# Optimization experiments

Hardware: AMD Instinct MI355X
Metric: run time of the kernel (lower is better)

## Reference

```python
import jax, jax.numpy as jnp
import numpy as np

E = 6            # number of residual adapter experts / event groups
MAX_SCALE = 0.05
RESIDUAL_SCALE = 1.0
EPS = 1e-12      # F.normalize eps


def setup_inputs() -> dict:
    key = jax.random.key(0)
    ks = jax.random.split(key, 8)
    B, L, D, H, T = 4, 1024, 768, 1536, 32
    seq_embeddings = jax.random.normal(ks[0], (B, L, D), dtype=jnp.float32)
    next_type_ids = jax.random.randint(ks[1], (B, L), 0, T, dtype=jnp.int32)
    # Adapter bank params (6 two-layer MLPs). Original zero-inits W2/b2; we use
    # small random values so the math is exercised.
    W1 = jax.random.normal(ks[2], (E, D, H), dtype=jnp.float32) * 0.02
    b1 = jax.random.normal(ks[3], (E, H), dtype=jnp.float32) * 0.02
    W2 = jax.random.normal(ks[4], (E, H, D), dtype=jnp.float32) * 0.02
    b2 = jax.random.normal(ks[5], (E, D), dtype=jnp.float32) * 0.02
    raw_alpha = jnp.full((E,), -4.0, dtype=jnp.float32)
    # build_event_type_to_group_tensor stand-in: event type -> one of 6 groups
    event_type_to_group = (jnp.arange(T, dtype=jnp.int32) % E)
    return {"seq_embeddings": seq_embeddings, "next_type_ids": next_type_ids,
            "W1": W1, "b1": b1, "W2": W2, "b2": b2,
            "raw_alpha": raw_alpha, "event_type_to_group": event_type_to_group}


def reference(seq_embeddings, next_type_ids, W1, b1, W2, b2, raw_alpha, event_type_to_group):
    x = seq_embeddings                                  # [B, L, D]
    T = event_type_to_group.shape[0]
    safe = jnp.clip(next_type_ids.astype(jnp.int32), 0, T - 1)
    group_ids = event_type_to_group[safe]               # [B, L] in [0, 6)
    # Dense compute of all 6 adapters (dropout is identity in eval mode)
    h = jax.nn.relu(jnp.einsum('bld,edh->bleh', x, W1) + b1)   # [B, L, 6, H]
    residuals = jnp.einsum('bleh,ehd->bled', h, W2) + b2       # [B, L, 6, D]
    # Gather the chosen expert's residual per token
    idx = group_ids[..., None, None]                           # [B, L, 1, 1]
    residual = jnp.take_along_axis(residuals, idx, axis=2)[:, :, 0, :]  # [B, L, D]
    alpha_all = MAX_SCALE * jax.nn.sigmoid(raw_alpha)          # [6]
    alpha = alpha_all[group_ids][..., None]                    # [B, L, 1]
    out = x + RESIDUAL_SCALE * alpha * residual
    norm = jnp.linalg.norm(out, axis=-1, keepdims=True)
    out = out / jnp.maximum(norm, EPS)
    return out
```

## Files before the change

### kernel.cpp

```cpp
#include <hip/hip_runtime.h>
#include <hip/hip_bf16.h>
#include <stdint.h>

#define NTOK 4096
#define DDIM 768
#define HDIM 1536
#define NEXP 6
#define NTYPE 32
#define PADROWS 4224
#define MAXTILES 70

typedef __bf16 bf16x8 __attribute__((ext_vector_type(8)));
typedef float f32x4 __attribute__((ext_vector_type(4)));

static __device__ __forceinline__ unsigned short f2bf(float f) {
  union { float f; unsigned u; } v; v.f = f;
  unsigned r = v.u + 0x7FFFu + ((v.u >> 16) & 1u);
  return (unsigned short)(r >> 16);
}

static __device__ __forceinline__ void gload_lds16(const void* g, void* lds) {
  auto* g1 = reinterpret_cast<const __attribute__((address_space(1))) uint32_t*>(
      reinterpret_cast<uintptr_t>(g));
  auto* l3 = reinterpret_cast<__attribute__((address_space(3))) uint32_t*>(
      (uint32_t)reinterpret_cast<uintptr_t>(lds));
  __builtin_amdgcn_global_load_lds(g1, l3, 16, 0, 0);
}

__global__ __launch_bounds__(256)
void prep_kernel(const float* __restrict__ W1, const float* __restrict__ W2,
                 unsigned short* __restrict__ w1t, unsigned short* __restrict__ w2t,
                 const int* __restrict__ ids, const int* __restrict__ ev2g,
                 int* __restrict__ perm, int* __restrict__ meta) {
  const int z = blockIdx.z;
  const int t = threadIdx.x;
  if (z == 12) {
    if (blockIdx.x != 0 || blockIdx.y != 0) return;
    __shared__ int s_ev2g[NTYPE];
    __shared__ int s_cnt[NEXP];
    __shared__ int s_off[NEXP];
    __shared__ int s_cur[NEXP];
    if (t < NTYPE) s_ev2g[t] = ev2g[t];
    if (t < NEXP) { s_cnt[t] = 0; s_cur[t] = 0; }
    __syncthreads();
    int g[16];
    #pragma unroll
    for (int i = 0; i < 16; ++i) {
      int idx = t * 16 + i;
      int ty = ids[idx];
      ty = ty < 0 ? 0 : (ty > NTYPE - 1 ? NTYPE - 1 : ty);
      g[i] = s_ev2g[ty];
      atomicAdd(&s_cnt[g[i]], 1);
    }
    __syncthreads();
    if (t == 0) {
      int off = 0, nt = 0;
      int* table = meta + 21;
      for (int e = 0; e < NEXP; ++e) {
        s_off[e] = off;
        int c = s_cnt[e];
        for (int k = 0; k * 64 < c; ++k) {
          int rem = c - k * 64;
          table[nt * 3 + 0] = e;
          table[nt * 3 + 1] = off + k * 64;
          table[nt * 3 + 2] = rem < 64 ? rem : 64;
          ++nt;
        }
        off += c;
      }
      meta[20] = nt;
    }
    __syncthreads();
    #pragma unroll
    for (int i = 0; i < 16; ++i) {
      int idx = t * 16 + i;
      int pos = s_off[g[i]] + atomicAdd(&s_cur[g[i]], 1);
      perm[pos] = idx;
    }
    return;
  }
  __shared__ float tile[64][65];
  const float* src;
  unsigned short* dst;
  int R, C, bx, by;
  if (z < 6) {
    src = W1 + (size_t)z * 768 * 1536; dst = w1t + (size_t)z * 768 * 1536;
    R = 768; C = 1536; bx = blockIdx.x; by = blockIdx.y;
  } else {
    src = W2 + (size_t)(z - 6) * 768 * 1536; dst = w2t + (size_t)(z - 6) * 768 * 1536;
    R = 1536; C = 768; bx = blockIdx.y; by = blockIdx.x;
  }
  const int r0 = by * 64, c0 = bx * 64;
  const int lr = t >> 4;
  const int lc = (t & 15) << 2;
  #pragma unroll
  for (int i = 0; i < 4; ++i) {
    float4 v = *reinterpret_cast<const float4*>(src + (size_t)(r0 + i * 16 + lr) * C + c0 + lc);
    tile[i * 16 + lr][lc]     = v.x;
    tile[i * 16 + lr][lc + 1] = v.y;
    tile[i * 16 + lr][lc + 2] = v.z;
    tile[i * 16 + lr][lc + 3] = v.w;
  }
  __syncthreads();
  const int l8 = (t & 7) << 3;
  #pragma unroll
  for (int p = 0; p < 2; ++p) {
    int j = p * 32 + (t >> 3);
    union { unsigned short u[8]; uint4 v; } pk;
    #pragma unroll
    for (int k = 0; k < 8; ++k) pk.u[k] = f2bf(tile[l8 + k][j]);
    *reinterpret_cast<uint4*>(dst + (size_t)(c0 + j) * R + r0 + l8) = pk.v;
  }
}

__global__ __launch_bounds__(256)
void xgather_kernel(const float* __restrict__ x, const int* __restrict__ perm,
                    unsigned short* __restrict__ xg) {
  const int wave = threadIdx.x >> 6, lane = threadIdx.x & 63;
  const int row = (blockIdx.x << 2) + wave;
  const int src = perm[row];
  const float4* in = reinterpret_cast<const float4*>(x + (size_t)src * DDIM);
  ushort4* outp = reinterpret_cast<ushort4*>(xg + (size_t)row * DDIM);
  #pragma unroll
  for (int j = 0; j < 3; ++j) {
    float4 v = in[lane + j * 64];
    ushort4 o;
    o.x = f2bf(v.x); o.y = f2bf(v.y); o.z = f2bf(v.z); o.w = f2bf(v.w);
    outp[lane + j * 64] = o;
  }
}

template <int K, int NT, bool PASS2>
__global__ __launch_bounds__(256, 3)
void gemm_kernel(const unsigned short* __restrict__ A,
                 const unsigned short* __restrict__ Bw,
                 const float* __restrict__ bias,
                 const int* __restrict__ meta,
                 const int* __restrict__ perm,
                 const float* __restrict__ x,
                 const float* __restrict__ raw_alpha,
                 unsigned short* __restrict__ hout,
                 float* __restrict__ out)
{
  constexpr int BM = 64, BN = 128;
  constexpr int NDIM = NT * BN;
  constexpr int NK = K / 64;

  const int nwg = MAXTILES * NT;
  const int q = nwg >> 3, r = nwg & 7;
  const int x8 = blockIdx.x & 7;
  const int o8 = blockIdx.x >> 3;
  const int vid = (x8 < r ? x8 * (q + 1) : r * (q + 1) + (x8 - r) * q) + o8;
  const int nt = vid / MAXTILES;
  const int mt = vid % MAXTILES;
  if (mt >= meta[20]) return;
  const int* table = meta + 21;
  const int e = table[mt * 3 + 0], base = table[mt * 3 + 1], cnt = table[mt * 3 + 2];

  __shared__ __align__(16) unsigned short As[2][BM * 64];
  __shared__ __align__(16) unsigned short Bs[2][BN * 64];

  const int tid = threadIdx.x;
  const int wave = tid >> 6, lane = tid & 63;
  const int wm = wave >> 1, wn = wave & 1;

  const unsigned short* Abase = A + (size_t)base * K;
  const unsigned short* Bbase = Bw + ((size_t)e * NDIM + (size_t)nt * BN) * K;

  f32x4 acc[2][4];
  #pragma unroll
  for (int i = 0; i < 2; ++i)
    #pragma unroll
    for (int j = 0; j < 4; ++j) acc[i][j] = (f32x4){0.f, 0.f, 0.f, 0.f};

  int aRow[2], aElem[2], aLds[2];
  #pragma unroll
  for (int i = 0; i < 2; ++i) {
    int chunk = i * 256 + tid;
    int o = chunk * 16;
    int row = o >> 7;
    int inb = (o & 127) ^ ((row & 7) << 4);
    aRow[i] = row; aElem[i] = inb >> 1;
    aLds[i] = (i * 256 + wave * 64) * 16;
  }
  int bRow[4], bElem[4], bLds[4];
  #pragma unroll
  for (int i = 0; i < 4; ++i) {
    int chunk = i * 256 + tid;
    int o = chunk * 16;
    int row = o >> 7;
    int inb = (o & 127) ^ ((row & 7) << 4);
    bRow[i] = row; bElem[i] = inb >> 1;
    bLds[i] = (i * 256 + wave * 64) * 16;
  }

  #pragma unroll
  for (int i = 0; i < 2; ++i)
    gload_lds16(Abase + (size_t)aRow[i] * K + aElem[i], (char*)As[0] + aLds[i]);
  #pragma unroll
  for (int i = 0; i < 4; ++i)
    gload_lds16(Bbase + (size_t)bRow[i] * K + bElem[i], (char*)Bs[0] + bLds[i]);
  __syncthreads();

  int cur = 0;
  for (int kt = 0; kt < NK; ++kt) {
    if (kt + 1 < NK) {
      const int k0 = (kt + 1) * 64;
      #pragma unroll
      for (int i = 0; i < 2; ++i)
        gload_lds16(Abase + (size_t)aRow[i] * K + k0 + aElem[i], (char*)As[cur ^ 1] + aLds[i]);
      #pragma unroll
      for (int i = 0; i < 4; ++i)
        gload_lds16(Bbase + (size_t)bRow[i] * K + k0 + bElem[i], (char*)Bs[cur ^ 1] + bLds[i]);
    }
    #pragma unroll
    for (int ks = 0; ks < 2; ++ks) {
      bf16x8 av[2], bv[4];
      const int kb = ks * 64 + ((lane >> 4) << 4);
      #pragma unroll
      for (int mi = 0; mi < 2; ++mi) {
        int row = wm * 32 + mi * 16 + (lane & 15);
        int byte = (row * 128 + kb) ^ ((row & 7) << 4);
        av[mi] = *reinterpret_cast<const bf16x8*>((const char*)As[cur] + byte);
      }
      #pragma unroll
      for (int nj = 0; nj < 4; ++nj) {
        int row = wn * 64 + nj * 16 + (lane & 15);
        int byte = (row * 128 + kb) ^ ((row & 7) << 4);
        bv[nj] = *reinterpret_cast<const bf16x8*>((const char*)Bs[cur] + byte);
      }
      #pragma unroll
      for (int mi = 0; mi < 2; ++mi)
        #pragma unroll
        for (int nj = 0; nj < 4; ++nj)
          acc[mi][nj] = __builtin_amdgcn_mfma_f32_16x16x32_bf16(av[mi], bv[nj], acc[mi][nj], 0, 0, 0);
    }
    __syncthreads();
    cur ^= 1;
  }

  const int col0 = nt * BN + wn * 64;
  if constexpr (!PASS2) {
    #pragma unroll
    for (int nj = 0; nj < 4; ++nj) {
      int n = col0 + nj * 16 + (lane & 15);
      float bv = bias[e * NDIM + n];
      #pragma unroll
      for (int mi = 0; mi < 2; ++mi) {
        int rbase = wm * 32 + mi * 16 + ((lane >> 4) << 2);
        #pragma unroll
        for (int rr = 0; rr < 4; ++rr) {
          int row = rbase + rr;
          if (row < cnt) {
            float v = fmaxf(acc[mi][nj][rr] + bv, 0.0f);
            hout[(size_t)(base + row) * NDIM + n] = f2bf(v);
          }
        }
      }
    }
  } else {
    float alpha = 0.05f / (1.0f + expf(-raw_alpha[e]));
    #pragma unroll
    for (int nj = 0; nj < 4; ++nj) {
      int n = col0 + nj * 16 + (lane & 15);
      float bv = bias[e * NDIM + n];
      #pragma unroll
      for (int mi = 0; mi < 2; ++mi) {
        int rbase = wm * 32 + mi * 16 + ((lane >> 4) << 2);
        #pragma unroll
        for (int rr = 0; rr < 4; ++rr) {
          int row = rbase + rr;
          if (row < cnt) {
            int tok = perm[base + row];
            size_t oi = (size_t)tok * DDIM + n;
            out[oi] = x[oi] + alpha * (acc[mi][nj][rr] + bv);
          }
        }
      }
    }
  }
}

__global__ __launch_bounds__(256)
void norm_kernel(float* __restrict__ out) {
  const int wave = threadIdx.x >> 6, lane = threadIdx.x & 63;
  const int tok = (blockIdx.x << 2) + wave;
  float4* p = reinterpret_cast<float4*>(out) + (size_t)tok * 192;
  float4 a = p[lane], b = p[lane + 64], c = p[lane + 128];
  float ss = a.x * a.x + a.y * a.y + a.z * a.z + a.w * a.w
           + b.x * b.x + b.y * b.y + b.z * b.z + b.w * b.w
           + c.x * c.x + c.y * c.y + c.z * c.z + c.w * c.w;
  #pragma unroll
  for (int off = 32; off; off >>= 1) ss += __shfl_xor(ss, off);
  const float s = 1.0f / fmaxf(sqrtf(ss), 1e-12f);
  a.x *= s; a.y *= s; a.z *= s; a.w *= s;
  b.x *= s; b.y *= s; b.z *= s; b.w *= s;
  c.x *= s; c.y *= s; c.z *= s; c.w *= s;
  p[lane] = a; p[lane + 64] = b; p[lane + 128] = c;
}


extern "C" void kernel_launch(void* const* d_in, const int* in_sizes, int n_in,
                              void* d_out, int out_size, void* d_ws, size_t ws_size,
                              hipStream_t stream) {
  const float* x      = (const float*)d_in[0];
  const int*   ids    = (const int*)d_in[1];
  const float* W1     = (const float*)d_in[2];
  const float* b1     = (const float*)d_in[3];
  const float* W2     = (const float*)d_in[4];
  const float* b2     = (const float*)d_in[5];
  const float* ralpha = (const float*)d_in[6];
  const int*   ev2g   = (const int*)d_in[7];
  float* out = (float*)d_out;
  char* ws = (char*)d_ws;

  unsigned short* w1t = (unsigned short*)(ws);
  unsigned short* w2t = (unsigned short*)(ws + 14155776);
  unsigned short* xg  = (unsigned short*)(ws + 28311552);
  unsigned short* h   = (unsigned short*)(ws + 34799616);
  int* perm = (int*)(ws + 47775744);
  int* meta = (int*)(ws + 47808512);

  prep_kernel<<<dim3(24, 12, 13), 256, 0, stream>>>(W1, W2, w1t, w2t, ids, ev2g, perm, meta);
  xgather_kernel<<<1024, 256, 0, stream>>>(x, perm, xg);
  gemm_kernel<DDIM, 12, false><<<MAXTILES * 12, 256, 0, stream>>>(
      xg, w1t, b1, meta, perm, x, ralpha, h, out);
  gemm_kernel<HDIM, 6, true><<<MAXTILES * 6, 256, 0, stream>>>(
      h, w2t, b2, meta, perm, x, ralpha, nullptr, out);
  norm_kernel<<<1024, 256, 0, stream>>>(out);
}
```

Measured before the change: 186.2 us.

## Triple-buffer GEMM LDS tiles with explicit vmcnt waits for deeper prefetch

Converts the double-buffered global-to-LDS pipeline in the expert GEMM into a three-stage ring that prefetches two K tiles ahead. Manual s_waitcnt vmcnt counts and raw s_barrier calls replace __syncthreads, so the kernel waits only for the tile about to be consumed. This is meant to hide more global load latency behind MFMA work. In exchange, LDS use per block grows by half and the occupancy hint drops from 3 to 2 blocks per CU. The hard-coded vmcnt values assume exactly six loads per stage.

```diff
diff --git a/kernel.cpp b/kernel.cpp
--- a/kernel.cpp
+++ b/kernel.cpp
@@ -131,7 +131,7 @@
 }
 
 template <int K, int NT, bool PASS2>
-__global__ __launch_bounds__(256, 3)
+__global__ __launch_bounds__(256, 2)
 void gemm_kernel(const unsigned short* __restrict__ A,
                  const unsigned short* __restrict__ Bw,
                  const float* __restrict__ bias,
@@ -157,8 +157,8 @@
   const int* table = meta + 21;
   const int e = table[mt * 3 + 0], base = table[mt * 3 + 1], cnt = table[mt * 3 + 2];
 
-  __shared__ __align__(16) unsigned short As[2][BM * 64];
-  __shared__ __align__(16) unsigned short Bs[2][BN * 64];
+  __shared__ __align__(16) unsigned short As[3][BM * 64];
+  __shared__ __align__(16) unsigned short Bs[3][BN * 64];
 
   const int tid = threadIdx.x;
   const int wave = tid >> 6, lane = tid & 63;
@@ -194,25 +194,28 @@
     bLds[i] = (i * 256 + wave * 64) * 16;
   }
 
-  #pragma unroll
-  for (int i = 0; i < 2; ++i)
-    gload_lds16(Abase + (size_t)aRow[i] * K + aElem[i], (char*)As[0] + aLds[i]);
-  #pragma unroll
-  for (int i = 0; i < 4; ++i)
-    gload_lds16(Bbase + (size_t)bRow[i] * K + bElem[i], (char*)Bs[0] + bLds[i]);
-  __syncthreads();
-
-  int cur = 0;
+  auto stage = [&](int kt, int buf) {
+    const int k0 = kt * 64;
+    #pragma unroll
+    for (int i = 0; i < 2; ++i)
+      gload_lds16(Abase + (size_t)aRow[i] * K + k0 + aElem[i], (char*)As[buf] + aLds[i]);
+    #pragma unroll
+    for (int i = 0; i < 4; ++i)
+      gload_lds16(Bbase + (size_t)bRow[i] * K + k0 + bElem[i], (char*)Bs[buf] + bLds[i]);
+  };
+
+  stage(0, 0);
+  stage(1, 1);
+
+  int get = 0, put = 2;
   for (int kt = 0; kt < NK; ++kt) {
-    if (kt + 1 < NK) {
-      const int k0 = (kt + 1) * 64;
-      #pragma unroll
-      for (int i = 0; i < 2; ++i)
-        gload_lds16(Abase + (size_t)aRow[i] * K + k0 + aElem[i], (char*)As[cur ^ 1] + aLds[i]);
-      #pragma unroll
-      for (int i = 0; i < 4; ++i)
-        gload_lds16(Bbase + (size_t)bRow[i] * K + k0 + bElem[i], (char*)Bs[cur ^ 1] + bLds[i]);
-    }
+    if (kt + 2 < NK) stage(kt + 2, put);
+    __builtin_amdgcn_sched_barrier(0);
+    if (kt + 2 < NK)      asm volatile("s_waitcnt vmcnt(12)" ::: "memory");
+    else if (kt + 1 < NK) asm volatile("s_waitcnt vmcnt(6)" ::: "memory");
+    else                  asm volatile("s_waitcnt vmcnt(0)" ::: "memory");
+    __builtin_amdgcn_s_barrier();
+    __builtin_amdgcn_sched_barrier(0);
     #pragma unroll
     for (int ks = 0; ks < 2; ++ks) {
       bf16x8 av[2], bv[4];
@@ -221,13 +224,13 @@
       for (int mi = 0; mi < 2; ++mi) {
         int row = wm * 32 + mi * 16 + (lane & 15);
         int byte = (row * 128 + kb) ^ ((row & 7) << 4);
-        av[mi] = *reinterpret_cast<const bf16x8*>((const char*)As[cur] + byte);
+        av[mi] = *reinterpret_cast<const bf16x8*>((const char*)As[get] + byte);
       }
       #pragma unroll
       for (int nj = 0; nj < 4; ++nj) {
         int row = wn * 64 + nj * 16 + (lane & 15);
         int byte = (row * 128 + kb) ^ ((row & 7) << 4);
-        bv[nj] = *reinterpret_cast<const bf16x8*>((const char*)Bs[cur] + byte);
+        bv[nj] = *reinterpret_cast<const bf16x8*>((const char*)Bs[get] + byte);
       }
       #pragma unroll
       for (int mi = 0; mi < 2; ++mi)
@@ -235,8 +238,10 @@
         for (int nj = 0; nj < 4; ++nj)
           acc[mi][nj] = __builtin_amdgcn_mfma_f32_16x16x32_bf16(av[mi], bv[nj], acc[mi][nj], 0, 0, 0);
     }
-    __syncthreads();
-    cur ^= 1;
+    __builtin_amdgcn_sched_barrier(0);
+    __builtin_amdgcn_s_barrier();
+    get = (get == 2) ? 0 : get + 1;
+    put = (put == 2) ? 0 : put + 1;
   }
 
   const int col0 = nt * BN + wn * 64;
```

Result: no change. 185.0 us (-0.6%).
